# Kernel optimization log

Hardware: AMD Instinct MI355X
Metric: run time of the kernel (lower is better)

## Reference

```python
import math
import jax, jax.numpy as jnp
import numpy as np

HEADS = 16


def setup_inputs() -> dict:
    key = jax.random.key(0)
    k1, k2, k3 = jax.random.split(key, 3)
    bs, n_ctx, width = 2, 2048, 1024
    x = jax.random.normal(k1, (bs, n_ctx, width), dtype=jnp.float32)
    # init_scale=0.25 style small init for stability
    W_qkv = jax.random.normal(k2, (width, 3 * width), dtype=jnp.float32) * (0.25 / math.sqrt(width))
    b_qkv = jnp.zeros((3 * width,), dtype=jnp.float32)
    W_proj = jax.random.normal(k3, (width, width), dtype=jnp.float32) * (0.25 / math.sqrt(width))
    b_proj = jnp.zeros((width,), dtype=jnp.float32)
    return {"x": x, "W_qkv": W_qkv, "b_qkv": b_qkv, "W_proj": W_proj, "b_proj": b_proj}


def reference(x, W_qkv, b_qkv, W_proj, b_proj):
    bs, n_ctx, width = x.shape
    qkv = x @ W_qkv + b_qkv                     # [b, s, 3*width]
    attn_ch = width // HEADS                    # head dim
    qkv = qkv.reshape(bs, n_ctx, HEADS, 3 * attn_ch)
    q, k, v = jnp.split(qkv, 3, axis=-1)        # each [b, s, h, c]
    scale = 1.0 / math.sqrt(math.sqrt(attn_ch)) # applied to both q and k
    weight = jnp.einsum('bthc,bshc->bhts', q * scale, k * scale)
    weight = jax.nn.softmax(weight.astype(jnp.float32), axis=-1).astype(qkv.dtype)
    out = jnp.einsum('bhts,bshc->bthc', weight, v).reshape(bs, n_ctx, width)
    return out @ W_proj + b_proj
```

## Files before the change

kernel.cpp:

```cpp
#include <hip/hip_runtime.h>


using u16 = unsigned short;
typedef __attribute__((ext_vector_type(8))) short s16x8;
typedef __attribute__((ext_vector_type(4))) float f32x4;
typedef __attribute__((ext_vector_type(16))) float f32x16;

__device__ __forceinline__ u16 f2bf(float f) {
    unsigned x = __builtin_bit_cast(unsigned, f);
    x += 0x7fffu + ((x >> 16) & 1u);
    return (u16)(x >> 16);
}
__device__ __forceinline__ float bf2f(u16 u) {
    return __builtin_bit_cast(float, ((unsigned)u) << 16);
}
__device__ __forceinline__ unsigned pk2bf(float lo, float hi) {
    unsigned a = __builtin_bit_cast(unsigned, lo);
    unsigned b = __builtin_bit_cast(unsigned, hi);
    a += 0x7fffu + ((a >> 16) & 1u);
    b += 0x7fffu + ((b >> 16) & 1u);
    return (a >> 16) | (b & 0xffff0000u);
}

#define MFMA(a, b, c)   __builtin_amdgcn_mfma_f32_16x16x32_bf16((a), (b), (c), 0, 0, 0)
#define MFMA32(a, b, c) __builtin_amdgcn_mfma_f32_32x32x16_bf16((a), (b), (c), 0, 0, 0)


__global__ __launch_bounds__(256) void convert_split(const float* __restrict__ in,
                                                     u16* __restrict__ H, u16* __restrict__ L, int n) {
    int i = (blockIdx.x * 256 + threadIdx.x) * 4;
    if (i >= n) return;
    float4 v = *(const float4*)(in + i);
    u16 h0 = f2bf(v.x), h1 = f2bf(v.y), h2 = f2bf(v.z), h3 = f2bf(v.w);
    ushort4 hh = { h0, h1, h2, h3 };
    ushort4 ll = { f2bf(v.x - bf2f(h0)), f2bf(v.y - bf2f(h1)), f2bf(v.z - bf2f(h2)), f2bf(v.w - bf2f(h3)) };
    *(ushort4*)(H + i) = hh;
    *(ushort4*)(L + i) = ll;
}

__global__ __launch_bounds__(256) void transpose_split(const float* __restrict__ W,
                                                       u16* __restrict__ TH, u16* __restrict__ TL,
                                                       int K, int N) {
    __shared__ float st[32][33];
    int n0 = blockIdx.x * 32, k0 = blockIdx.y * 32;
    int c = threadIdx.x & 31, r8 = threadIdx.x >> 5;
#pragma unroll
    for (int i = 0; i < 4; ++i) {
        int r = r8 + i * 8;
        st[r][c] = W[(size_t)(k0 + r) * N + n0 + c];
    }
    __syncthreads();
#pragma unroll
    for (int i = 0; i < 4; ++i) {
        int r = r8 + i * 8;
        float v = st[c][r];
        u16 h = f2bf(v);
        TH[(size_t)(n0 + r) * K + k0 + c] = h;
        TL[(size_t)(n0 + r) * K + k0 + c] = f2bf(v - bf2f(h));
    }
}


template <int EPI>
__global__ __launch_bounds__(256, 2) void gemm_bf16x3(
    const u16* __restrict__ AH, const u16* __restrict__ AL,
    const u16* __restrict__ BTH, const u16* __restrict__ BTL,
    const float* __restrict__ bias,
    u16* __restrict__ Qs, u16* __restrict__ Kb, u16* __restrict__ Vp,
    float* __restrict__ Out) {
    const int K = 1024;
    __shared__ u16 sAh[128][40], sAl[128][40], sBh[128][40], sBl[128][40];

    int m0 = blockIdx.y * 128, n0 = blockIdx.x * 128;
    int tid = threadIdx.x, lane = tid & 63, wv = tid >> 6;
    int g = lane >> 4, c16 = lane & 15;
    int wm = wv >> 1, wn = wv & 1;

    f32x4 acc[4][4] = {};

    for (int kt = 0; kt < 32; ++kt) {
        int k0 = kt * 32;
        s16x8 ra[2], rla[2], rb[2], rlb[2];
#pragma unroll
        for (int i = 0; i < 2; ++i) {
            int cc = i * 256 + tid;
            int rr = cc >> 2, ko = (cc & 3) * 8;
            ra[i]  = *(const s16x8*)(AH  + (size_t)(m0 + rr) * K + k0 + ko);
            rla[i] = *(const s16x8*)(AL  + (size_t)(m0 + rr) * K + k0 + ko);
            rb[i]  = *(const s16x8*)(BTH + (size_t)(n0 + rr) * K + k0 + ko);
            rlb[i] = *(const s16x8*)(BTL + (size_t)(n0 + rr) * K + k0 + ko);
        }
        __syncthreads();
#pragma unroll
        for (int i = 0; i < 2; ++i) {
            int cc = i * 256 + tid;
            int rr = cc >> 2, ko = (cc & 3) * 8;
            *(s16x8*)&sAh[rr][ko] = ra[i];
            *(s16x8*)&sAl[rr][ko] = rla[i];
            *(s16x8*)&sBh[rr][ko] = rb[i];
            *(s16x8*)&sBl[rr][ko] = rlb[i];
        }
        __syncthreads();

        s16x8 ah[4], al[4], bh[4], bl[4];
#pragma unroll
        for (int mi = 0; mi < 4; ++mi) {
            ah[mi] = *(const s16x8*)&sAh[wm * 64 + mi * 16 + c16][g * 8];
            al[mi] = *(const s16x8*)&sAl[wm * 64 + mi * 16 + c16][g * 8];
        }
#pragma unroll
        for (int ni = 0; ni < 4; ++ni) {
            bh[ni] = *(const s16x8*)&sBh[wn * 64 + ni * 16 + c16][g * 8];
            bl[ni] = *(const s16x8*)&sBl[wn * 64 + ni * 16 + c16][g * 8];
        }
#pragma unroll
        for (int mi = 0; mi < 4; ++mi)
#pragma unroll
            for (int ni = 0; ni < 4; ++ni) {
                f32x4 c = acc[mi][ni];
                c = MFMA(ah[mi], bh[ni], c);
                c = MFMA(al[mi], bh[ni], c);
                c = MFMA(ah[mi], bl[ni], c);
                acc[mi][ni] = c;
            }
    }

#pragma unroll
    for (int ni = 0; ni < 4; ++ni) {
        int col = n0 + wn * 64 + ni * 16 + c16;
        float bs = bias[col];
        if (EPI == 0) {
            int h = col / 192;
            int rm = col - h * 192;
#pragma unroll
            for (int mi = 0; mi < 4; ++mi)
#pragma unroll
                for (int r = 0; r < 4; ++r) {
                    int row = m0 + wm * 64 + mi * 16 + 4 * g + r;
                    int b = row >> 11, s = row & 2047;
                    int bh16 = b * 16 + h;
                    float val = acc[mi][ni][r] + bs;
                    if (rm < 64)
                        Qs[(((size_t)bh16 * 2048 + s) << 6) + rm] = f2bf(val * 0.18033688011112042f);
                    else if (rm < 128)
                        Kb[(((size_t)bh16 * 2048 + s) << 6) + rm - 64] = f2bf(val);
                    else {
                        int d = rm - 128;
                        int kg = s >> 4, k16 = s & 15;
                        int mm = (k16 & 3) | (((k16 >> 3) & 1) << 2) | (((k16 >> 2) & 1) << 3);
                        Vp[(((size_t)bh16 * 128 + kg) * 64 + d) * 16 + mm] = f2bf(val);
                    }
                }
        } else {
#pragma unroll
            for (int mi = 0; mi < 4; ++mi)
#pragma unroll
                for (int r = 0; r < 4; ++r) {
                    int row = m0 + wm * 64 + mi * 16 + 4 * g + r;
                    Out[(size_t)row * 1024 + col] = acc[mi][ni][r] + bs;
                }
        }
    }
}

__global__ __launch_bounds__(256, 2) void attn_fwd(
    const u16* __restrict__ Qs, const u16* __restrict__ Kb, const u16* __restrict__ Vp,
    u16* __restrict__ OH, u16* __restrict__ OL) {
    int id = blockIdx.x;
    int xcd = id & 7, li = id >> 3;
    int bh = xcd * 4 + (li >> 4);
    int qb = li & 15;
    int tid = threadIdx.x, w = tid >> 6, lane = tid & 63;
    int l31 = lane & 31, h = lane >> 5;
    int q0 = (qb * 4 + w) * 32;

    size_t base = (size_t)bh * 2048 * 64;
    size_t vbase = (size_t)bh * 131072;

    const u16* qp = Qs + base + (size_t)(q0 + l31) * 64 + 8 * h;
    s16x8 qf[4];
#pragma unroll
    for (int c = 0; c < 4; ++c) qf[c] = *(const s16x8*)(qp + 16 * c);

    const u16* kp = Kb + base + (size_t)l31 * 64 + 8 * h;
    const u16* vb = Vp + vbase + (size_t)l31 * 16 + 8 * h;

    f32x16 o0 = {}, o1 = {};
    float m = -1e30f, ls = 0.f;

    s16x8 kA[8], kB[8];
#pragma unroll
    for (int i = 0; i < 8; ++i)
        kA[i] = *(const s16x8*)(kp + (i >> 2) * 2048 + (i & 3) * 16);

    auto step = [&](s16x8 (&cur)[8], s16x8 (&nxt)[8], int j) {
        const u16* vp = vb + (size_t)j * 4096;
        s16x8 v[8];
#pragma unroll
        for (int b = 0; b < 2; ++b)
#pragma unroll
            for (int hf = 0; hf < 2; ++hf)
#pragma unroll
                for (int n = 0; n < 2; ++n)
                    v[b * 4 + hf * 2 + n] = *(const s16x8*)(vp + b * 2048 + hf * 1024 + n * 512);

        f32x16 s0 = {}, s1 = {};
        s0 = MFMA32(cur[0], qf[0], s0);
        s0 = MFMA32(cur[1], qf[1], s0);
        s0 = MFMA32(cur[2], qf[2], s0);
        s0 = MFMA32(cur[3], qf[3], s0);
        s1 = MFMA32(cur[4], qf[0], s1);
        s1 = MFMA32(cur[5], qf[1], s1);
        s1 = MFMA32(cur[6], qf[2], s1);
        s1 = MFMA32(cur[7], qf[3], s1);

        int jn = (j + 1) & 31;
        const u16* kpn = kp + (size_t)jn * 4096;
#pragma unroll
        for (int i = 0; i < 8; ++i)
            nxt[i] = *(const s16x8*)(kpn + (i >> 2) * 2048 + (i & 3) * 16);

        float t0 = fmaxf(s0[0], s1[0]), t1 = fmaxf(s0[1], s1[1]);
        float t2 = fmaxf(s0[2], s1[2]), t3 = fmaxf(s0[3], s1[3]);
#pragma unroll
        for (int r = 4; r < 16; r += 4) {
            t0 = fmaxf(t0, fmaxf(s0[r], s1[r]));
            t1 = fmaxf(t1, fmaxf(s0[r + 1], s1[r + 1]));
            t2 = fmaxf(t2, fmaxf(s0[r + 2], s1[r + 2]));
            t3 = fmaxf(t3, fmaxf(s0[r + 3], s1[r + 3]));
        }
        float pmax = fmaxf(fmaxf(t0, t1), fmaxf(t2, t3));
        pmax = fmaxf(pmax, __shfl_xor(pmax, 32));

        if (!__all(pmax <= m + 8.f)) {
            float mn = fmaxf(m, pmax);
            float f = __builtin_amdgcn_exp2f(m - mn);
            m = mn;
            ls *= f;
#pragma unroll
            for (int r = 0; r < 16; ++r) {
                float fb = __shfl(f, (r & 3) + 8 * (r >> 2) + 4 * h);
                o0[r] *= fb;
                o1[r] *= fb;
            }
        }

        float a0 = 0.f, a1 = 0.f, a2 = 0.f, a3 = 0.f;
#pragma unroll
        for (int r = 0; r < 16; r += 4) {
            s0[r]     = __builtin_amdgcn_exp2f(s0[r] - m);     a0 += s0[r];
            s0[r + 1] = __builtin_amdgcn_exp2f(s0[r + 1] - m); a1 += s0[r + 1];
            s0[r + 2] = __builtin_amdgcn_exp2f(s0[r + 2] - m); a2 += s0[r + 2];
            s0[r + 3] = __builtin_amdgcn_exp2f(s0[r + 3] - m); a3 += s0[r + 3];
            s1[r]     = __builtin_amdgcn_exp2f(s1[r] - m);     a0 += s1[r];
            s1[r + 1] = __builtin_amdgcn_exp2f(s1[r + 1] - m); a1 += s1[r + 1];
            s1[r + 2] = __builtin_amdgcn_exp2f(s1[r + 2] - m); a2 += s1[r + 2];
            s1[r + 3] = __builtin_amdgcn_exp2f(s1[r + 3] - m); a3 += s1[r + 3];
        }
        float sm = (a0 + a1) + (a2 + a3);
        sm += __shfl_xor(sm, 32);
        ls += sm;

        union { s16x8 v8; unsigned u[4]; } p00, p01, p10, p11;
#pragma unroll
        for (int k = 0; k < 4; ++k) {
            p00.u[k] = pk2bf(s0[2 * k], s0[2 * k + 1]);
            p01.u[k] = pk2bf(s0[8 + 2 * k], s0[9 + 2 * k]);
            p10.u[k] = pk2bf(s1[2 * k], s1[2 * k + 1]);
            p11.u[k] = pk2bf(s1[8 + 2 * k], s1[9 + 2 * k]);
        }

        o0 = MFMA32(p00.v8, v[0], o0);
        o1 = MFMA32(p00.v8, v[1], o1);
        o0 = MFMA32(p01.v8, v[2], o0);
        o1 = MFMA32(p01.v8, v[3], o1);
        o0 = MFMA32(p10.v8, v[4], o0);
        o1 = MFMA32(p10.v8, v[5], o1);
        o0 = MFMA32(p11.v8, v[6], o0);
        o1 = MFMA32(p11.v8, v[7], o1);
    };

    for (int j = 0; j < 32; j += 2) {
        step(kA, kB, j);
        step(kB, kA, j + 1);
    }

    int b = bh >> 4, hh = bh & 15;
    float inv = 1.0f / ls;
#pragma unroll
    for (int r = 0; r < 16; ++r) {
        int cr = (r & 3) + 8 * (r >> 2) + 4 * h;
        float fb = __shfl(inv, cr);
        int row = q0 + cr;
        size_t idx = ((size_t)(b * 2048 + row)) * 1024 + hh * 64 + l31;
        float v0 = o0[r] * fb, v1 = o1[r] * fb;
        u16 h0 = f2bf(v0);
        OH[idx] = h0;
        OL[idx] = f2bf(v0 - bf2f(h0));
        u16 h1 = f2bf(v1);
        OH[idx + 32] = h1;
        OL[idx + 32] = f2bf(v1 - bf2f(h1));
    }
}


extern "C" void kernel_launch(void* const* d_in, const int* in_sizes, int n_in,
                              void* d_out, int out_size, void* d_ws, size_t ws_size,
                              hipStream_t stream) {
    const float* x     = (const float*)d_in[0];
    const float* Wqkv  = (const float*)d_in[1];
    const float* bqkv  = (const float*)d_in[2];
    const float* Wproj = (const float*)d_in[3];
    const float* bproj = (const float*)d_in[4];
    float* out = (float*)d_out;

    char* w = (char*)d_ws;
    const size_t SZ_X  = (size_t)4096 * 1024 * 2;
    const size_t SZ_WQ = (size_t)3072 * 1024 * 2;
    const size_t SZ_WP = (size_t)1024 * 1024 * 2;
    u16* XH  = (u16*)w; w += SZ_X;
    u16* XL  = (u16*)w; w += SZ_X;
    u16* WQH = (u16*)w; w += SZ_WQ;
    u16* WQL = (u16*)w; w += SZ_WQ;
    u16* WPH = (u16*)w; w += SZ_WP;
    u16* WPL = (u16*)w; w += SZ_WP;
    u16* Q_s = (u16*)w; w += SZ_X;
    u16* K_b = (u16*)w; w += SZ_X;
    u16* V_p = (u16*)w; w += SZ_X;
    u16* OHp = (u16*)w; w += SZ_X;
    u16* OLp = (u16*)w; w += SZ_X;

    convert_split<<<4096, 256, 0, stream>>>(x, XH, XL, 4096 * 1024);
    transpose_split<<<dim3(96, 32), 256, 0, stream>>>(Wqkv, WQH, WQL, 1024, 3072);
    transpose_split<<<dim3(32, 32), 256, 0, stream>>>(Wproj, WPH, WPL, 1024, 1024);
    gemm_bf16x3<0><<<dim3(24, 32), 256, 0, stream>>>(XH, XL, WQH, WQL, bqkv, Q_s, K_b, V_p, nullptr);
    attn_fwd<<<512, 256, 0, stream>>>(Q_s, K_b, V_p, OHp, OLp);
    gemm_bf16x3<1><<<dim3(8, 32), 256, 0, stream>>>(OHp, OLp, WPH, WPL, bproj, nullptr, nullptr, nullptr, out);
}
```

Measured before the change: 216.6 us.

## Split attention KV range across two wave groups and merge via LDS

Doubles the attention block to 512 threads, with each pair of waves handling the same 32 query rows but separate halves of the key/value sequence. The partial outputs, maxima and sums are combined through shared memory with a log-sum-exp rescale before the bf16 hi/lo split and store. It also raises wave priority around MFMA groups with s_setprio. The aim is more waves per CU and shorter serial KV loops per wave, at the cost of an LDS reduction, a barrier and higher register pressure under launch_bounds(512,4).

```diff
diff --git a/kernel.cpp b/kernel.cpp
--- a/kernel.cpp
+++ b/kernel.cpp
@@ -163,16 +163,20 @@
     }
 }
 
-__global__ __launch_bounds__(256, 2) void attn_fwd(
+__global__ __launch_bounds__(512, 4) void attn_fwd(
     const u16* __restrict__ Qs, const u16* __restrict__ Kb, const u16* __restrict__ Vp,
     u16* __restrict__ OH, u16* __restrict__ OL) {
+    __shared__ float Lo[4][64][33];
+    __shared__ float Lm[4][32], Ll[4][32];
+
     int id = blockIdx.x;
     int xcd = id & 7, li = id >> 3;
     int bh = xcd * 4 + (li >> 4);
     int qb = li & 15;
     int tid = threadIdx.x, w = tid >> 6, lane = tid & 63;
     int l31 = lane & 31, h = lane >> 5;
-    int q0 = (qb * 4 + w) * 32;
+    int qs = w & 3, kvh = w >> 2;
+    int q0 = (qb * 4 + qs) * 32;
 
     size_t base = (size_t)bh * 2048 * 64;
     size_t vbase = (size_t)bh * 131072;
@@ -188,12 +192,14 @@
     f32x16 o0 = {}, o1 = {};
     float m = -1e30f, ls = 0.f;
 
+    const int j0 = kvh * 16;
+
     s16x8 kA[8], kB[8];
 #pragma unroll
     for (int i = 0; i < 8; ++i)
-        kA[i] = *(const s16x8*)(kp + (i >> 2) * 2048 + (i & 3) * 16);
-
-    auto step = [&](s16x8 (&cur)[8], s16x8 (&nxt)[8], int j) {
+        kA[i] = *(const s16x8*)(kp + (size_t)j0 * 4096 + (i >> 2) * 2048 + (i & 3) * 16);
+
+    auto step = [&](s16x8 (&cur)[8], s16x8 (&nxt)[8], int j, int jn) {
         const u16* vp = vb + (size_t)j * 4096;
         s16x8 v[8];
 #pragma unroll
@@ -205,6 +211,7 @@
                     v[b * 4 + hf * 2 + n] = *(const s16x8*)(vp + b * 2048 + hf * 1024 + n * 512);
 
         f32x16 s0 = {}, s1 = {};
+        __builtin_amdgcn_s_setprio(1);
         s0 = MFMA32(cur[0], qf[0], s0);
         s0 = MFMA32(cur[1], qf[1], s0);
         s0 = MFMA32(cur[2], qf[2], s0);
@@ -213,8 +220,8 @@
         s1 = MFMA32(cur[5], qf[1], s1);
         s1 = MFMA32(cur[6], qf[2], s1);
         s1 = MFMA32(cur[7], qf[3], s1);
-
-        int jn = (j + 1) & 31;
+        __builtin_amdgcn_s_setprio(0);
+
         const u16* kpn = kp + (size_t)jn * 4096;
 #pragma unroll
         for (int i = 0; i < 8; ++i)
@@ -270,6 +277,7 @@
             p11.u[k] = pk2bf(s1[8 + 2 * k], s1[9 + 2 * k]);
         }
 
+        __builtin_amdgcn_s_setprio(1);
         o0 = MFMA32(p00.v8, v[0], o0);
         o1 = MFMA32(p00.v8, v[1], o1);
         o0 = MFMA32(p01.v8, v[2], o0);
@@ -278,28 +286,48 @@
         o1 = MFMA32(p10.v8, v[5], o1);
         o0 = MFMA32(p11.v8, v[6], o0);
         o1 = MFMA32(p11.v8, v[7], o1);
+        __builtin_amdgcn_s_setprio(0);
     };
 
-    for (int j = 0; j < 32; j += 2) {
-        step(kA, kB, j);
-        step(kB, kA, j + 1);
-    }
-
-    int b = bh >> 4, hh = bh & 15;
-    float inv = 1.0f / ls;
-#pragma unroll
-    for (int r = 0; r < 16; ++r) {
-        int cr = (r & 3) + 8 * (r >> 2) + 4 * h;
-        float fb = __shfl(inv, cr);
-        int row = q0 + cr;
-        size_t idx = ((size_t)(b * 2048 + row)) * 1024 + hh * 64 + l31;
-        float v0 = o0[r] * fb, v1 = o1[r] * fb;
-        u16 h0 = f2bf(v0);
-        OH[idx] = h0;
-        OL[idx] = f2bf(v0 - bf2f(h0));
-        u16 h1 = f2bf(v1);
-        OH[idx + 32] = h1;
-        OL[idx + 32] = f2bf(v1 - bf2f(h1));
+    for (int jj = 0; jj < 16; jj += 2) {
+        step(kA, kB, j0 + jj, j0 + ((jj + 1) & 15));
+        step(kB, kA, j0 + jj + 1, j0 + ((jj + 2) & 15));
+    }
+
+    if (w >= 4) {
+        int wp = w - 4;
+        if (lane < 32) { Lm[wp][lane] = m; Ll[wp][lane] = ls; }
+#pragma unroll
+        for (int r = 0; r < 16; ++r) {
+            Lo[wp][lane][r] = o0[r];
+            Lo[wp][lane][16 + r] = o1[r];
+        }
+    }
+    __syncthreads();
+    if (w < 4) {
+        float m_b = Lm[w][l31], ls_b = Ll[w][l31];
+        float mt = fmaxf(m, m_b);
+        float sa = __builtin_amdgcn_exp2f(m - mt);
+        float sb = __builtin_amdgcn_exp2f(m_b - mt);
+        float inv = 1.0f / (ls * sa + ls_b * sb);
+        float ca = sa * inv, cb = sb * inv;
+        int b = bh >> 4, hh = bh & 15;
+#pragma unroll
+        for (int r = 0; r < 16; ++r) {
+            int cr = (r & 3) + 8 * (r >> 2) + 4 * h;
+            float fa = __shfl(ca, cr);
+            float fc = __shfl(cb, cr);
+            int row = q0 + cr;
+            size_t idx = ((size_t)(b * 2048 + row)) * 1024 + hh * 64 + l31;
+            float v0 = o0[r] * fa + Lo[w][lane][r] * fc;
+            float v1 = o1[r] * fa + Lo[w][lane][16 + r] * fc;
+            u16 h0 = f2bf(v0);
+            OH[idx] = h0;
+            OL[idx] = f2bf(v0 - bf2f(h0));
+            u16 h1 = f2bf(v1);
+            OH[idx + 32] = h1;
+            OL[idx + 32] = f2bf(v1 - bf2f(h1));
+        }
     }
 }
 
@@ -334,6 +362,6 @@
     transpose_split<<<dim3(96, 32), 256, 0, stream>>>(Wqkv, WQH, WQL, 1024, 3072);
     transpose_split<<<dim3(32, 32), 256, 0, stream>>>(Wproj, WPH, WPL, 1024, 1024);
     gemm_bf16x3<0><<<dim3(24, 32), 256, 0, stream>>>(XH, XL, WQH, WQL, bqkv, Q_s, K_b, V_p, nullptr);
-    attn_fwd<<<512, 256, 0, stream>>>(Q_s, K_b, V_p, OHp, OLp);
+    attn_fwd<<<512, 512, 0, stream>>>(Q_s, K_b, V_p, OHp, OLp);
     gemm_bf16x3<1><<<dim3(8, 32), 256, 0, stream>>>(OHp, OLp, WPH, WPL, bproj, nullptr, nullptr, nullptr, out);
 }
```

New measurement: 380.4 us. 75.6% more time.

## Stage K/V tiles in shared memory via global_load_lds double buffering

Applied to the files above, without the earlier changes.

Before, each of the four waves loaded its own full K and V tiles from global memory into registers. Now the block loads each K/V tile once, with the waves splitting the work, into a double-buffered LDS array using global_load_lds, and every wave reads its fragments from LDS. This cuts duplicate global/L2 traffic by four and frees registers. In exchange it adds a __syncthreads per iteration and LDS read latency, and it wraps the MFMA blocks in s_setprio hints.

```diff
diff --git a/kernel.cpp b/kernel.cpp
--- a/kernel.cpp
+++ b/kernel.cpp
@@ -20,6 +20,11 @@
     a += 0x7fffu + ((a >> 16) & 1u);
     b += 0x7fffu + ((b >> 16) & 1u);
     return (a >> 16) | (b & 0xffff0000u);
+}
+__device__ __forceinline__ void gll16(const void* g, void* l) {
+    __builtin_amdgcn_global_load_lds(
+        (const __attribute__((address_space(1))) unsigned int*)g,
+        (__attribute__((address_space(3))) unsigned int*)l, 16, 0, 0);
 }
 
 #define MFMA(a, b, c)   __builtin_amdgcn_mfma_f32_16x16x32_bf16((a), (b), (c), 0, 0, 0)
@@ -166,13 +171,15 @@
 __global__ __launch_bounds__(256, 2) void attn_fwd(
     const u16* __restrict__ Qs, const u16* __restrict__ Kb, const u16* __restrict__ Vp,
     u16* __restrict__ OH, u16* __restrict__ OL) {
+    __shared__ u16 sKV[2][16][512];
+
     int id = blockIdx.x;
     int xcd = id & 7, li = id >> 3;
     int bh = xcd * 4 + (li >> 4);
-    int qb = li & 15;
+    int qblk = li & 15;
     int tid = threadIdx.x, w = tid >> 6, lane = tid & 63;
     int l31 = lane & 31, h = lane >> 5;
-    int q0 = (qb * 4 + w) * 32;
+    int q0 = (qblk * 4 + w) * 32;
 
     size_t base = (size_t)bh * 2048 * 64;
     size_t vbase = (size_t)bh * 131072;
@@ -182,43 +189,49 @@
 #pragma unroll
     for (int c = 0; c < 4; ++c) qf[c] = *(const s16x8*)(qp + 16 * c);
 
-    const u16* kp = Kb + base + (size_t)l31 * 64 + 8 * h;
-    const u16* vb = Vp + vbase + (size_t)l31 * 16 + 8 * h;
+    const int pk0 = 2 * w, pk1 = 2 * w + 1;
+    const u16* gk0 = Kb + base + (size_t)((pk0 >> 2) * 32 + l31) * 64 + 16 * (pk0 & 3) + 8 * h;
+    const u16* gk1 = Kb + base + (size_t)((pk1 >> 2) * 32 + l31) * 64 + 16 * (pk1 & 3) + 8 * h;
+    const u16* gv0 = Vp + vbase + (size_t)pk0 * 512 + (size_t)l31 * 16 + 8 * h;
+    const u16* gv1 = Vp + vbase + (size_t)pk1 * 512 + (size_t)l31 * 16 + 8 * h;
+
+    auto stage = [&](int buf, int jj) {
+        size_t ko = (size_t)jj * 4096;
+        gll16(gk0 + ko, &sKV[buf][pk0][0]);
+        gll16(gk1 + ko, &sKV[buf][pk1][0]);
+        gll16(gv0 + ko, &sKV[buf][8 + pk0][0]);
+        gll16(gv1 + ko, &sKV[buf][8 + pk1][0]);
+    };
 
     f32x16 o0 = {}, o1 = {};
     float m = -1e30f, ls = 0.f;
-
-    s16x8 kA[8], kB[8];
-#pragma unroll
-    for (int i = 0; i < 8; ++i)
-        kA[i] = *(const s16x8*)(kp + (i >> 2) * 2048 + (i & 3) * 16);
-
-    auto step = [&](s16x8 (&cur)[8], s16x8 (&nxt)[8], int j) {
-        const u16* vp = vb + (size_t)j * 4096;
-        s16x8 v[8];
-#pragma unroll
-        for (int b = 0; b < 2; ++b)
-#pragma unroll
-            for (int hf = 0; hf < 2; ++hf)
-#pragma unroll
-                for (int n = 0; n < 2; ++n)
-                    v[b * 4 + hf * 2 + n] = *(const s16x8*)(vp + b * 2048 + hf * 1024 + n * 512);
+    const int lo = lane * 8;
+
+    stage(0, 0);
+
+    for (int jj = 0; jj < 32; ++jj) {
+        int cur = jj & 1;
+        __syncthreads();
+        if (jj < 31) stage(cur ^ 1, jj + 1);
+
+        s16x8 kf[8], vf[8];
+#pragma unroll
+        for (int i = 0; i < 8; ++i) {
+            kf[i] = *(const s16x8*)&sKV[cur][i][lo];
+            vf[i] = *(const s16x8*)&sKV[cur][8 + i][lo];
+        }
 
         f32x16 s0 = {}, s1 = {};
-        s0 = MFMA32(cur[0], qf[0], s0);
-        s0 = MFMA32(cur[1], qf[1], s0);
-        s0 = MFMA32(cur[2], qf[2], s0);
-        s0 = MFMA32(cur[3], qf[3], s0);
-        s1 = MFMA32(cur[4], qf[0], s1);
-        s1 = MFMA32(cur[5], qf[1], s1);
-        s1 = MFMA32(cur[6], qf[2], s1);
-        s1 = MFMA32(cur[7], qf[3], s1);
-
-        int jn = (j + 1) & 31;
-        const u16* kpn = kp + (size_t)jn * 4096;
-#pragma unroll
-        for (int i = 0; i < 8; ++i)
-            nxt[i] = *(const s16x8*)(kpn + (i >> 2) * 2048 + (i & 3) * 16);
+        __builtin_amdgcn_s_setprio(1);
+        s0 = MFMA32(kf[0], qf[0], s0);
+        s0 = MFMA32(kf[1], qf[1], s0);
+        s0 = MFMA32(kf[2], qf[2], s0);
+        s0 = MFMA32(kf[3], qf[3], s0);
+        s1 = MFMA32(kf[4], qf[0], s1);
+        s1 = MFMA32(kf[5], qf[1], s1);
+        s1 = MFMA32(kf[6], qf[2], s1);
+        s1 = MFMA32(kf[7], qf[3], s1);
+        __builtin_amdgcn_s_setprio(0);
 
         float t0 = fmaxf(s0[0], s1[0]), t1 = fmaxf(s0[1], s1[1]);
         float t2 = fmaxf(s0[2], s1[2]), t3 = fmaxf(s0[3], s1[3]);
@@ -270,19 +283,16 @@
             p11.u[k] = pk2bf(s1[8 + 2 * k], s1[9 + 2 * k]);
         }
 
-        o0 = MFMA32(p00.v8, v[0], o0);
-        o1 = MFMA32(p00.v8, v[1], o1);
-        o0 = MFMA32(p01.v8, v[2], o0);
-        o1 = MFMA32(p01.v8, v[3], o1);
-        o0 = MFMA32(p10.v8, v[4], o0);
-        o1 = MFMA32(p10.v8, v[5], o1);
-        o0 = MFMA32(p11.v8, v[6], o0);
-        o1 = MFMA32(p11.v8, v[7], o1);
-    };
-
-    for (int j = 0; j < 32; j += 2) {
-        step(kA, kB, j);
-        step(kB, kA, j + 1);
+        __builtin_amdgcn_s_setprio(1);
+        o0 = MFMA32(p00.v8, vf[0], o0);
+        o1 = MFMA32(p00.v8, vf[1], o1);
+        o0 = MFMA32(p01.v8, vf[2], o0);
+        o1 = MFMA32(p01.v8, vf[3], o1);
+        o0 = MFMA32(p10.v8, vf[4], o0);
+        o1 = MFMA32(p10.v8, vf[5], o1);
+        o0 = MFMA32(p11.v8, vf[6], o0);
+        o1 = MFMA32(p11.v8, vf[7], o1);
+        __builtin_amdgcn_s_setprio(0);
     }
 
     int b = bh >> 4, hh = bh & 15;
```

After: 194.2 us (median of 2 runs). -10.4%, faster.
